# Kernel tuning notes

Measured on AMD Instinct MI355X. Metric: run time of the kernel, lower is better.

## Reference

```python
import jax, jax.numpy as jnp
import numpy as np
import math

SEQ_LEN = 2048
EMB = 1024
HEAD = 64
BATCH = 8

def setup_inputs() -> dict:
    key = jax.random.key(0)
    k1, k2, k3, k4 = jax.random.split(key, 4)
    x = jax.random.normal(k1, (BATCH, SEQ_LEN, EMB), dtype=jnp.float32)
    # torch Linear(no bias): out = x @ W.T with W [out,in]; store as [in,out]
    s = 1.0 / math.sqrt(EMB)
    Wk = jax.random.uniform(k2, (EMB, HEAD), dtype=jnp.float32, minval=-s, maxval=s)
    Wq = jax.random.uniform(k3, (EMB, HEAD), dtype=jnp.float32, minval=-s, maxval=s)
    Wv = jax.random.uniform(k4, (EMB, HEAD), dtype=jnp.float32, minval=-s, maxval=s)
    return {"x": x, "Wk": Wk, "Wq": Wq, "Wv": Wv}

def reference(x, Wk, Wq, Wv):
    B, S, E = x.shape
    H = Wk.shape[1]
    k = x @ Wk  # [B,S,H]
    q = x @ Wq
    v = x @ Wv
    scores = jnp.einsum('bsh,bth->bst', q, k) / math.sqrt(H)
    causal = jnp.tril(jnp.ones((S, S), dtype=bool))
    scores = jnp.where(causal[None], scores, -jnp.inf)
    attn = jax.nn.softmax(scores, axis=-1)
    # dropout is identity in eval mode
    return jnp.einsum('bst,bth->bsh', attn, v)
```

## Files before the change

kernel.cpp:

```cpp
#include <hip/hip_runtime.h>
#include <hip/hip_bf16.h>

typedef __attribute__((ext_vector_type(8))) short short8;
typedef __attribute__((ext_vector_type(4))) short short4v;
typedef __attribute__((ext_vector_type(4))) float floatx4;

#define SEQ   2048
#define EMB   1024
#define HEAD  64
#define BATCH 8

__device__ __forceinline__ short f2bf(float f) {
    union { float f; unsigned u; } a; a.f = f;
    return (short)((a.u + 0x8000u) >> 16);
}

__device__ __forceinline__ short8 pk8(floatx4 a, floatx4 b) {
    short8 r;
    #pragma unroll
    for (int i = 0; i < 4; ++i) {
        union { float f; unsigned u; } x1, x2;
        x1.f = a[i]; x2.f = b[i];
        r[i]     = (short)((x1.u + 0x8000u) >> 16);
        r[4 + i] = (short)((x2.u + 0x8000u) >> 16);
    }
    return r;
}

__device__ __forceinline__ void gld16(const void* g, void* l) {
    __builtin_amdgcn_global_load_lds(
        (const __attribute__((address_space(1))) unsigned int*)g,
        (__attribute__((address_space(3))) unsigned int*)l,
        16, 0, 0);
}

__global__ void wtrans_kernel(const float* __restrict__ Wk,
                              const float* __restrict__ Wq,
                              const float* __restrict__ Wv,
                              short* __restrict__ Wf) {
    int gid  = blockIdx.x * 256 + threadIdx.x;
    int lane = gid & 63;
    int fid  = gid >> 6;
    int chunk = fid & 31;
    int mnt  = fid >> 5;
    int mat  = mnt >> 2, nt = mnt & 3;
    const float* src = (mat == 0) ? Wq : (mat == 1) ? Wk : Wv;
    int n = lane & 15, quad = lane >> 4;
    int h = nt * 16 + n;
    short8 o8;
    #pragma unroll
    for (int j = 0; j < 8; ++j)
        o8[j] = f2bf(src[(chunk * 32 + quad * 8 + j) * 64 + h]);
    *(short8*)(Wf + (long)gid * 8) = o8;
}

__global__ __launch_bounds__(256, 1) void qkv_kernel(const float* __restrict__ x,
                                                     const short* __restrict__ Wf,
                                                     short* __restrict__ q,
                                                     short* __restrict__ k,
                                                     short* __restrict__ vt) {
    __shared__ short LW[2][12][4][64][8];
    const int wv   = threadIdx.x >> 6;
    const int lane = threadIdx.x & 63;
    const int l15  = lane & 15;
    const int quad = lane >> 4;
    const int rg   = wv >> 1;
    const int nh   = wv & 1;
    const int row0 = blockIdx.x * 64;

    floatx4 acc[12];
    #pragma unroll
    for (int f = 0; f < 12; ++f) acc[f] = (floatx4){0.f, 0.f, 0.f, 0.f};

    const float* xr0 = x + (long)(row0 + rg * 32 + l15) * EMB + quad * 8;
    const float* xr1 = xr0 + (long)16 * EMB;

    #pragma unroll
    for (int i = 0; i < 12; ++i) {
        const int s = wv * 12 + i, mnt = s >> 2, c = s & 3;
        gld16(Wf + (long)(mnt * 32 + c) * 512 + lane * 8, &LW[0][mnt][c][0][0]);
    }
    __syncthreads();

    #pragma unroll 1
    for (int g = 0; g < 8; ++g) {
        const int bb = g & 1;
        floatx4 xv[16];
        #pragma unroll
        for (int c = 0; c < 4; ++c) {
            const float* p0 = xr0 + g * 128 + c * 32;
            const float* p1 = xr1 + g * 128 + c * 32;
            xv[4 * c + 0] = *(const floatx4*)(p0);
            xv[4 * c + 1] = *(const floatx4*)(p0 + 4);
            xv[4 * c + 2] = *(const floatx4*)(p1);
            xv[4 * c + 3] = *(const floatx4*)(p1 + 4);
        }
        if (g < 7) {
            #pragma unroll
            for (int i = 0; i < 12; ++i) {
                const int s = wv * 12 + i, mnt = s >> 2, c = s & 3;
                gld16(Wf + (long)(mnt * 32 + (g + 1) * 4 + c) * 512 + lane * 8,
                      &LW[bb ^ 1][mnt][c][0][0]);
            }
        }
        #pragma unroll
        for (int c = 0; c < 4; ++c) {
            short8 a0 = pk8(xv[4 * c + 0], xv[4 * c + 1]);
            short8 a1 = pk8(xv[4 * c + 2], xv[4 * c + 3]);
            #pragma unroll
            for (int i = 0; i < 6; ++i) {
                short8 bf = *(const short8*)&LW[bb][nh * 6 + i][c][lane][0];
                acc[i]     = __builtin_amdgcn_mfma_f32_16x16x32_bf16(a0, bf, acc[i], 0, 0, 0);
                acc[6 + i] = __builtin_amdgcn_mfma_f32_16x16x32_bf16(a1, bf, acc[6 + i], 0, 0, 0);
            }
        }
        __syncthreads();
    }

    const int bidx = row0 >> 11;
    #pragma unroll
    for (int i = 0; i < 6; ++i) {
        const int mnt = nh * 6 + i;
        const int mat = mnt >> 2, ntl = mnt & 3;
        const int col = ntl * 16 + l15;
        #pragma unroll
        for (int rt = 0; rt < 2; ++rt) {
            const floatx4 av = acc[rt * 6 + i];
            const long rbase = row0 + rg * 32 + rt * 16 + quad * 4;
            if (mat == 0) {
                #pragma unroll
                for (int r = 0; r < 4; ++r)
                    q[(rbase + r) * HEAD + col] = f2bf(av[r]);
            } else if (mat == 1) {
                #pragma unroll
                for (int r = 0; r < 4; ++r)
                    k[(rbase + r) * HEAD + col] = f2bf(av[r]);
            } else {
                short4v vv;
                #pragma unroll
                for (int r = 0; r < 4; ++r) vv[r] = f2bf(av[r]);
                const int srow = (int)(rbase & (SEQ - 1));
                *(short4v*)(vt + ((long)bidx * HEAD + col) * SEQ + srow) = vv;
            }
        }
    }
}

__global__ __launch_bounds__(256, 2) void attn_kernel(const short* __restrict__ q,
                                                      const short* __restrict__ k,
                                                      const short* __restrict__ vt,
                                                      float* __restrict__ out) {
    __shared__ short KV[2][16][64][8];
    __shared__ short Plds[4][16][40];
    __shared__ float oT[2][2][16][64];
    __shared__ float lT[2][2][16];

    const int wv   = threadIdx.x >> 6;
    const int lane = threadIdx.x & 63;
    const int l15  = lane & 15;
    const int quad = lane >> 4;
    const int rg   = wv & 1;
    const int kh   = wv >> 1;
    const int b    = blockIdx.x & 7;
    const int p    = blockIdx.x >> 3;
    const int t2   = 63 - p;
    const int s1   = p * 32, s2 = t2 * 32;
    const int nch1 = (p >> 1) + 1;
    const int nch2 = (t2 >> 1) + 1;

    const short* kbase = k  + (long)b * SEQ * HEAD;
    const short* vbase = vt + (long)b * HEAD * SEQ;

    const short* q1p = q + ((long)b * SEQ + s1 + rg * 16 + l15) * HEAD + quad * 8;
    const short* q2p = q + ((long)b * SEQ + s2 + rg * 16 + l15) * HEAD + quad * 8;
    short8 q1f0 = *(const short8*)(q1p), q1f1 = *(const short8*)(q1p + 32);
    short8 q2f0 = *(const short8*)(q2p), q2f1 = *(const short8*)(q2p + 32);

    floatx4 o1[4], o2[4];
    #pragma unroll
    for (int nhh = 0; nhh < 4; ++nhh) {
        o1[nhh] = (floatx4){0.f, 0.f, 0.f, 0.f};
        o2[nhh] = (floatx4){0.f, 0.f, 0.f, 0.f};
    }
    float l1[4] = {0.f, 0.f, 0.f, 0.f};
    float l2[4] = {0.f, 0.f, 0.f, 0.f};

    auto stage = [&](int ch, int bb) {
        const int j0 = ch * 64;
        #pragma unroll
        for (int i = 0; i < 2; ++i) {
            const int fid = wv + i * 4;
            const int ntg = fid >> 1, ks = fid & 1;
            gld16(kbase + (long)(j0 + ntg * 16 + l15) * HEAD + ks * 32 + quad * 8,
                  &KV[bb][fid][0][0]);
        }
        #pragma unroll
        for (int i = 0; i < 2; ++i) {
            const int fid = wv + i * 4;
            const int kh2 = fid >> 2, nth = fid & 3;
            gld16(vbase + (long)(nth * 16 + l15) * SEQ + j0 + kh2 * 32 + quad * 8,
                  &KV[bb][8 + fid][0][0]);
        }
    };

    stage(0, 0);
    __syncthreads();

    #pragma unroll 1
    for (int ch = 0; ch < nch2; ++ch) {
        const int bb = ch & 1;
        if (ch + 1 < nch2) stage(ch + 1, bb ^ 1);
        const int j0 = ch * 64;

        short8 kf[2][2], vf[4];
        #pragma unroll
        for (int nt = 0; nt < 2; ++nt)
            #pragma unroll
            for (int ks = 0; ks < 2; ++ks)
                kf[nt][ks] = *(const short8*)&KV[bb][(kh * 2 + nt) * 2 + ks][lane][0];
        #pragma unroll
        for (int nhh = 0; nhh < 4; ++nhh)
            vf[nhh] = *(const short8*)&KV[bb][8 + kh * 4 + nhh][lane][0];

        {
            floatx4 sa[2];
            sa[0] = (floatx4){0.f, 0.f, 0.f, 0.f};
            sa[1] = (floatx4){0.f, 0.f, 0.f, 0.f};
            #pragma unroll
            for (int nt = 0; nt < 2; ++nt) {
                sa[nt] = __builtin_amdgcn_mfma_f32_16x16x32_bf16(q2f0, kf[nt][0], sa[nt], 0, 0, 0);
                sa[nt] = __builtin_amdgcn_mfma_f32_16x16x32_bf16(q2f1, kf[nt][1], sa[nt], 0, 0, 0);
            }
            #pragma unroll
            for (int r = 0; r < 4; ++r) {
                const int sq = s2 + rg * 16 + quad * 4 + r;
                #pragma unroll
                for (int nt = 0; nt < 2; ++nt) {
                    const int sk = j0 + kh * 32 + nt * 16 + l15;
                    float pv = (sk > sq) ? 0.f : __expf(sa[nt][r] * 0.125f - 16.f);
                    sa[nt][r] = pv;
                    l2[r] += pv;
                }
            }
            #pragma unroll
            for (int nt = 0; nt < 2; ++nt)
                #pragma unroll
                for (int r = 0; r < 4; ++r)
                    Plds[wv][quad * 4 + r][nt * 16 + l15] = f2bf(sa[nt][r]);
            short8 pf = *(const short8*)(&Plds[wv][l15][quad * 8]);
            #pragma unroll
            for (int nhh = 0; nhh < 4; ++nhh)
                o2[nhh] = __builtin_amdgcn_mfma_f32_16x16x32_bf16(pf, vf[nhh], o2[nhh], 0, 0, 0);
        }

        if (ch < nch1) {
            floatx4 sa[2];
            sa[0] = (floatx4){0.f, 0.f, 0.f, 0.f};
            sa[1] = (floatx4){0.f, 0.f, 0.f, 0.f};
            #pragma unroll
            for (int nt = 0; nt < 2; ++nt) {
                sa[nt] = __builtin_amdgcn_mfma_f32_16x16x32_bf16(q1f0, kf[nt][0], sa[nt], 0, 0, 0);
                sa[nt] = __builtin_amdgcn_mfma_f32_16x16x32_bf16(q1f1, kf[nt][1], sa[nt], 0, 0, 0);
            }
            #pragma unroll
            for (int r = 0; r < 4; ++r) {
                const int sq = s1 + rg * 16 + quad * 4 + r;
                #pragma unroll
                for (int nt = 0; nt < 2; ++nt) {
                    const int sk = j0 + kh * 32 + nt * 16 + l15;
                    float pv = (sk > sq) ? 0.f : __expf(sa[nt][r] * 0.125f - 16.f);
                    sa[nt][r] = pv;
                    l1[r] += pv;
                }
            }
            #pragma unroll
            for (int nt = 0; nt < 2; ++nt)
                #pragma unroll
                for (int r = 0; r < 4; ++r)
                    Plds[wv][quad * 4 + r][nt * 16 + l15] = f2bf(sa[nt][r]);
            short8 pf = *(const short8*)(&Plds[wv][l15][quad * 8]);
            #pragma unroll
            for (int nhh = 0; nhh < 4; ++nhh)
                o1[nhh] = __builtin_amdgcn_mfma_f32_16x16x32_bf16(pf, vf[nhh], o1[nhh], 0, 0, 0);
        }
        __syncthreads();
    }

    #pragma unroll
    for (int msk = 1; msk <= 8; msk <<= 1) {
        #pragma unroll
        for (int r = 0; r < 4; ++r) {
            l1[r] += __shfl_xor(l1[r], msk, 64);
            l2[r] += __shfl_xor(l2[r], msk, 64);
        }
    }

    if (kh == 1) {
        #pragma unroll
        for (int nhh = 0; nhh < 4; ++nhh)
            #pragma unroll
            for (int r = 0; r < 4; ++r) {
                oT[0][rg][quad * 4 + r][nhh * 16 + l15] = o1[nhh][r];
                oT[1][rg][quad * 4 + r][nhh * 16 + l15] = o2[nhh][r];
            }
        if (l15 == 0) {
            #pragma unroll
            for (int r = 0; r < 4; ++r) {
                lT[0][rg][quad * 4 + r] = l1[r];
                lT[1][rg][quad * 4 + r] = l2[r];
            }
        }
    }
    __syncthreads();
    if (kh == 0) {
        #pragma unroll
        for (int r = 0; r < 4; ++r) {
            const int row = quad * 4 + r;
            const float inv1 = 1.f / (l1[r] + lT[0][rg][row]);
            const float inv2 = 1.f / (l2[r] + lT[1][rg][row]);
            #pragma unroll
            for (int nhh = 0; nhh < 4; ++nhh) {
                const int col = nhh * 16 + l15;
                out[((long)b * SEQ + s1 + rg * 16 + row) * HEAD + col] =
                    (o1[nhh][r] + oT[0][rg][row][col]) * inv1;
                out[((long)b * SEQ + s2 + rg * 16 + row) * HEAD + col] =
                    (o2[nhh][r] + oT[1][rg][row][col]) * inv2;
            }
        }
    }
}

extern "C" void kernel_launch(void* const* d_in, const int* in_sizes, int n_in,
                              void* d_out, int out_size, void* d_ws, size_t ws_size,
                              hipStream_t stream) {
    const float* x  = (const float*)d_in[0];
    const float* Wk = (const float*)d_in[1];
    const float* Wq = (const float*)d_in[2];
    const float* Wv = (const float*)d_in[3];
    float* out = (float*)d_out;

    short* Wf = (short*)d_ws;
    short* q  = Wf + 3 * HEAD * EMB;
    short* k  = q + (long)BATCH * SEQ * HEAD;
    short* vt = k + (long)BATCH * SEQ * HEAD;

    hipLaunchKernelGGL(wtrans_kernel, dim3(96), dim3(256), 0, stream, Wk, Wq, Wv, Wf);
    hipLaunchKernelGGL(qkv_kernel, dim3(BATCH * SEQ / 64), dim3(256), 0, stream, x, Wf, q, k, vt);
    hipLaunchKernelGGL(attn_kernel, dim3(BATCH * 32), dim3(256), 0, stream, q, k, vt, out);
}
```

Before: 152.8 us.

## Split attention KV chunks across two wave groups with 512-thread blocks

```diff
diff --git a/kernel.cpp b/kernel.cpp
--- a/kernel.cpp
+++ b/kernel.cpp
@@ -146,21 +146,24 @@
     }
 }
 
-__global__ __launch_bounds__(256, 2) void attn_kernel(const short* __restrict__ q,
+__global__ __launch_bounds__(512, 2) void attn_kernel(const short* __restrict__ q,
                                                       const short* __restrict__ k,
                                                       const short* __restrict__ vt,
                                                       float* __restrict__ out) {
-    __shared__ short KV[2][16][64][8];
-    __shared__ short Plds[4][16][40];
-    __shared__ float oT[2][2][16][64];
-    __shared__ float lT[2][2][16];
-
-    const int wv   = threadIdx.x >> 6;
-    const int lane = threadIdx.x & 63;
+    __shared__ __align__(16) char smem[75776];
+    auto KV   = (short (*)[2][16][64][8])smem;
+    auto Plds = (short (*)[16][40])(smem + 65536);
+    float* oM = (float*)smem;
+    float* lM = (float*)(smem + 49152);
+
+    const int wv   = (int)threadIdx.x >> 6;
+    const int lane = (int)threadIdx.x & 63;
     const int l15  = lane & 15;
     const int quad = lane >> 4;
-    const int rg   = wv & 1;
-    const int kh   = wv >> 1;
+    const int ws   = wv & 3;
+    const int rg   = ws & 1;
+    const int kh   = ws >> 1;
+    const int par  = wv >> 2;
     const int b    = blockIdx.x & 7;
     const int p    = blockIdx.x >> 3;
     const int t2   = 63 - p;
@@ -189,99 +192,111 @@
         const int j0 = ch * 64;
         #pragma unroll
         for (int i = 0; i < 2; ++i) {
-            const int fid = wv + i * 4;
+            const int fid = ws + i * 4;
             const int ntg = fid >> 1, ks = fid & 1;
             gld16(kbase + (long)(j0 + ntg * 16 + l15) * HEAD + ks * 32 + quad * 8,
-                  &KV[bb][fid][0][0]);
+                  &KV[bb][par][fid][0][0]);
         }
         #pragma unroll
         for (int i = 0; i < 2; ++i) {
-            const int fid = wv + i * 4;
+            const int fid = ws + i * 4;
             const int kh2 = fid >> 2, nth = fid & 3;
             gld16(vbase + (long)(nth * 16 + l15) * SEQ + j0 + kh2 * 32 + quad * 8,
-                  &KV[bb][8 + fid][0][0]);
+                  &KV[bb][par][8 + fid][0][0]);
         }
     };
 
-    stage(0, 0);
+    stage(par, 0);
     __syncthreads();
 
+    const int ns = (nch2 + 1) >> 1;
     #pragma unroll 1
-    for (int ch = 0; ch < nch2; ++ch) {
-        const int bb = ch & 1;
-        if (ch + 1 < nch2) stage(ch + 1, bb ^ 1);
-        const int j0 = ch * 64;
-
-        short8 kf[2][2], vf[4];
-        #pragma unroll
-        for (int nt = 0; nt < 2; ++nt)
-            #pragma unroll
-            for (int ks = 0; ks < 2; ++ks)
-                kf[nt][ks] = *(const short8*)&KV[bb][(kh * 2 + nt) * 2 + ks][lane][0];
-        #pragma unroll
-        for (int nhh = 0; nhh < 4; ++nhh)
-            vf[nhh] = *(const short8*)&KV[bb][8 + kh * 4 + nhh][lane][0];
-
-        {
-            floatx4 sa[2];
-            sa[0] = (floatx4){0.f, 0.f, 0.f, 0.f};
-            sa[1] = (floatx4){0.f, 0.f, 0.f, 0.f};
-            #pragma unroll
-            for (int nt = 0; nt < 2; ++nt) {
-                sa[nt] = __builtin_amdgcn_mfma_f32_16x16x32_bf16(q2f0, kf[nt][0], sa[nt], 0, 0, 0);
-                sa[nt] = __builtin_amdgcn_mfma_f32_16x16x32_bf16(q2f1, kf[nt][1], sa[nt], 0, 0, 0);
-            }
-            #pragma unroll
-            for (int r = 0; r < 4; ++r) {
-                const int sq = s2 + rg * 16 + quad * 4 + r;
+    for (int t = 0; t < ns; ++t) {
+        const int bb = t & 1;
+        const int ch = 2 * t + par;
+        if (ch + 2 < nch2) stage(ch + 2, bb ^ 1);
+
+        if (ch < nch2) {
+            const int j0 = ch * 64;
+            short8 kf[2][2], vf[4];
+            #pragma unroll
+            for (int nt = 0; nt < 2; ++nt)
+                #pragma unroll
+                for (int ks = 0; ks < 2; ++ks)
+                    kf[nt][ks] = *(const short8*)&KV[bb][par][(kh * 2 + nt) * 2 + ks][lane][0];
+            #pragma unroll
+            for (int nhh = 0; nhh < 4; ++nhh)
+                vf[nhh] = *(const short8*)&KV[bb][par][8 + kh * 4 + nhh][lane][0];
+
+            {
+                floatx4 sa[2];
+                sa[0] = (floatx4){0.f, 0.f, 0.f, 0.f};
+                sa[1] = (floatx4){0.f, 0.f, 0.f, 0.f};
+                __builtin_amdgcn_s_setprio(1);
                 #pragma unroll
                 for (int nt = 0; nt < 2; ++nt) {
-                    const int sk = j0 + kh * 32 + nt * 16 + l15;
-                    float pv = (sk > sq) ? 0.f : __expf(sa[nt][r] * 0.125f - 16.f);
-                    sa[nt][r] = pv;
-                    l2[r] += pv;
-                }
-            }
-            #pragma unroll
-            for (int nt = 0; nt < 2; ++nt)
-                #pragma unroll
-                for (int r = 0; r < 4; ++r)
-                    Plds[wv][quad * 4 + r][nt * 16 + l15] = f2bf(sa[nt][r]);
-            short8 pf = *(const short8*)(&Plds[wv][l15][quad * 8]);
-            #pragma unroll
-            for (int nhh = 0; nhh < 4; ++nhh)
-                o2[nhh] = __builtin_amdgcn_mfma_f32_16x16x32_bf16(pf, vf[nhh], o2[nhh], 0, 0, 0);
-        }
-
-        if (ch < nch1) {
-            floatx4 sa[2];
-            sa[0] = (floatx4){0.f, 0.f, 0.f, 0.f};
-            sa[1] = (floatx4){0.f, 0.f, 0.f, 0.f};
-            #pragma unroll
-            for (int nt = 0; nt < 2; ++nt) {
-                sa[nt] = __builtin_amdgcn_mfma_f32_16x16x32_bf16(q1f0, kf[nt][0], sa[nt], 0, 0, 0);
-                sa[nt] = __builtin_amdgcn_mfma_f32_16x16x32_bf16(q1f1, kf[nt][1], sa[nt], 0, 0, 0);
-            }
-            #pragma unroll
-            for (int r = 0; r < 4; ++r) {
-                const int sq = s1 + rg * 16 + quad * 4 + r;
+                    sa[nt] = __builtin_amdgcn_mfma_f32_16x16x32_bf16(q2f0, kf[nt][0], sa[nt], 0, 0, 0);
+                    sa[nt] = __builtin_amdgcn_mfma_f32_16x16x32_bf16(q2f1, kf[nt][1], sa[nt], 0, 0, 0);
+                }
+                __builtin_amdgcn_s_setprio(0);
+                #pragma unroll
+                for (int r = 0; r < 4; ++r) {
+                    const int sq = s2 + rg * 16 + quad * 4 + r;
+                    #pragma unroll
+                    for (int nt = 0; nt < 2; ++nt) {
+                        const int sk = j0 + kh * 32 + nt * 16 + l15;
+                        float pv = (sk > sq) ? 0.f : __expf(sa[nt][r] * 0.125f - 16.f);
+                        sa[nt][r] = pv;
+                        l2[r] += pv;
+                    }
+                }
+                #pragma unroll
+                for (int nt = 0; nt < 2; ++nt)
+                    #pragma unroll
+                    for (int r = 0; r < 4; ++r)
+                        Plds[wv][quad * 4 + r][nt * 16 + l15] = f2bf(sa[nt][r]);
+                short8 pf = *(const short8*)(&Plds[wv][l15][quad * 8]);
+                __builtin_amdgcn_s_setprio(1);
+                #pragma unroll
+                for (int nhh = 0; nhh < 4; ++nhh)
+                    o2[nhh] = __builtin_amdgcn_mfma_f32_16x16x32_bf16(pf, vf[nhh], o2[nhh], 0, 0, 0);
+                __builtin_amdgcn_s_setprio(0);
+            }
+
+            if (ch < nch1) {
+                floatx4 sa[2];
+                sa[0] = (floatx4){0.f, 0.f, 0.f, 0.f};
+                sa[1] = (floatx4){0.f, 0.f, 0.f, 0.f};
+                __builtin_amdgcn_s_setprio(1);
                 #pragma unroll
                 for (int nt = 0; nt < 2; ++nt) {
-                    const int sk = j0 + kh * 32 + nt * 16 + l15;
-                    float pv = (sk > sq) ? 0.f : __expf(sa[nt][r] * 0.125f - 16.f);
-                    sa[nt][r] = pv;
-                    l1[r] += pv;
-                }
-            }
-            #pragma unroll
-            for (int nt = 0; nt < 2; ++nt)
-                #pragma unroll
-                for (int r = 0; r < 4; ++r)
-                    Plds[wv][quad * 4 + r][nt * 16 + l15] = f2bf(sa[nt][r]);
-            short8 pf = *(const short8*)(&Plds[wv][l15][quad * 8]);
-            #pragma unroll
-            for (int nhh = 0; nhh < 4; ++nhh)
-                o1[nhh] = __builtin_amdgcn_mfma_f32_16x16x32_bf16(pf, vf[nhh], o1[nhh], 0, 0, 0);
+                    sa[nt] = __builtin_amdgcn_mfma_f32_16x16x32_bf16(q1f0, kf[nt][0], sa[nt], 0, 0, 0);
+                    sa[nt] = __builtin_amdgcn_mfma_f32_16x16x32_bf16(q1f1, kf[nt][1], sa[nt], 0, 0, 0);
+                }
+                __builtin_amdgcn_s_setprio(0);
+                #pragma unroll
+                for (int r = 0; r < 4; ++r) {
+                    const int sq = s1 + rg * 16 + quad * 4 + r;
+                    #pragma unroll
+                    for (int nt = 0; nt < 2; ++nt) {
+                        const int sk = j0 + kh * 32 + nt * 16 + l15;
+                        float pv = (sk > sq) ? 0.f : __expf(sa[nt][r] * 0.125f - 16.f);
+                        sa[nt][r] = pv;
+                        l1[r] += pv;
+                    }
+                }
+                #pragma unroll
+                for (int nt = 0; nt < 2; ++nt)
+                    #pragma unroll
+                    for (int r = 0; r < 4; ++r)
+                        Plds[wv][quad * 4 + r][nt * 16 + l15] = f2bf(sa[nt][r]);
+                short8 pf = *(const short8*)(&Plds[wv][l15][quad * 8]);
+                __builtin_amdgcn_s_setprio(1);
+                #pragma unroll
+                for (int nhh = 0; nhh < 4; ++nhh)
+                    o1[nhh] = __builtin_amdgcn_mfma_f32_16x16x32_bf16(pf, vf[nhh], o1[nhh], 0, 0, 0);
+                __builtin_amdgcn_s_setprio(0);
+            }
         }
         __syncthreads();
     }
@@ -295,36 +310,49 @@
         }
     }
 
-    if (kh == 1) {
+    const int g = (par << 1) | kh;
+    if (g != 0) {
+        const int slot = g - 1;
         #pragma unroll
         for (int nhh = 0; nhh < 4; ++nhh)
             #pragma unroll
             for (int r = 0; r < 4; ++r) {
-                oT[0][rg][quad * 4 + r][nhh * 16 + l15] = o1[nhh][r];
-                oT[1][rg][quad * 4 + r][nhh * 16 + l15] = o2[nhh][r];
+                const int row = quad * 4 + r, col = nhh * 16 + l15;
+                oM[(((0 * 3 + slot) * 2 + rg) * 16 + row) * 64 + col] = o1[nhh][r];
+                oM[(((1 * 3 + slot) * 2 + rg) * 16 + row) * 64 + col] = o2[nhh][r];
             }
         if (l15 == 0) {
             #pragma unroll
             for (int r = 0; r < 4; ++r) {
-                lT[0][rg][quad * 4 + r] = l1[r];
-                lT[1][rg][quad * 4 + r] = l2[r];
+                lM[((0 * 3 + slot) * 2 + rg) * 16 + quad * 4 + r] = l1[r];
+                lM[((1 * 3 + slot) * 2 + rg) * 16 + quad * 4 + r] = l2[r];
             }
         }
     }
     __syncthreads();
-    if (kh == 0) {
+    if (g == 0) {
         #pragma unroll
         for (int r = 0; r < 4; ++r) {
             const int row = quad * 4 + r;
-            const float inv1 = 1.f / (l1[r] + lT[0][rg][row]);
-            const float inv2 = 1.f / (l2[r] + lT[1][rg][row]);
+            float ls1 = l1[r], ls2 = l2[r];
+            #pragma unroll
+            for (int slot = 0; slot < 3; ++slot) {
+                ls1 += lM[((0 * 3 + slot) * 2 + rg) * 16 + row];
+                ls2 += lM[((1 * 3 + slot) * 2 + rg) * 16 + row];
+            }
+            const float inv1 = 1.f / ls1;
+            const float inv2 = 1.f / ls2;
             #pragma unroll
             for (int nhh = 0; nhh < 4; ++nhh) {
                 const int col = nhh * 16 + l15;
-                out[((long)b * SEQ + s1 + rg * 16 + row) * HEAD + col] =
-                    (o1[nhh][r] + oT[0][rg][row][col]) * inv1;
-                out[((long)b * SEQ + s2 + rg * 16 + row) * HEAD + col] =
-                    (o2[nhh][r] + oT[1][rg][row][col]) * inv2;
+                float a1 = o1[nhh][r], a2 = o2[nhh][r];
+                #pragma unroll
+                for (int slot = 0; slot < 3; ++slot) {
+                    a1 += oM[(((0 * 3 + slot) * 2 + rg) * 16 + row) * 64 + col];
+                    a2 += oM[(((1 * 3 + slot) * 2 + rg) * 16 + row) * 64 + col];
+                }
+                out[((long)b * SEQ + s1 + rg * 16 + row) * HEAD + col] = a1 * inv1;
+                out[((long)b * SEQ + s2 + rg * 16 + row) * HEAD + col] = a2 * inv2;
             }
         }
     }
@@ -346,5 +374,5 @@
 
     hipLaunchKernelGGL(wtrans_kernel, dim3(96), dim3(256), 0, stream, Wk, Wq, Wv, Wf);
     hipLaunchKernelGGL(qkv_kernel, dim3(BATCH * SEQ / 64), dim3(256), 0, stream, x, Wf, q, k, vt);
-    hipLaunchKernelGGL(attn_kernel, dim3(BATCH * 32), dim3(256), 0, stream, q, k, vt, out);
-}
+    hipLaunchKernelGGL(attn_kernel, dim3(BATCH * 32), dim3(512), 0, stream, q, k, vt, out);
+}
```

Measured after the change: 142.2 us. 6.9% less time.
